# Performance work log

Measured on AMD Instinct MI355X. Metric: run time of the kernel, lower is better.

The kernel has to match this reference:

```python
import jax, jax.numpy as jnp
import numpy as np

POS_THR = 0.5
NEG_THR = 0.4
BBOX_STD = np.array([0.1, 0.1, 0.2, 0.2], dtype=np.float32)


def _make_boxes(key, shape, min_sz, max_sz):
    k1, k2, k3, k4 = jax.random.split(key, 4)
    cy = jax.random.uniform(k1, shape, minval=0.2, maxval=0.8)
    cx = jax.random.uniform(k2, shape, minval=0.2, maxval=0.8)
    h = jax.random.uniform(k3, shape, minval=min_sz, maxval=max_sz)
    w = jax.random.uniform(k4, shape, minval=min_sz, maxval=max_sz)
    return jnp.stack([cy - h * 0.5, cx - w * 0.5, cy + h * 0.5, cx + w * 0.5], axis=-1)


def setup_inputs() -> dict:
    key = jax.random.key(0)
    B, G, A = 16, 64, 65536
    kg, ka, kc = jax.random.split(key, 3)
    gt4 = _make_boxes(kg, (B, G), 0.05, 0.4)            # [B,G,4]
    n_valid = 20                                         # first n_valid gts valid, rest pad
    tag = (jnp.arange(G) < n_valid).astype(jnp.float32)
    tag = jnp.broadcast_to(tag, (B, G))
    gt_boxes = jnp.concatenate([gt4, tag[..., None]], axis=-1)          # [B,G,5]
    cls = jax.random.randint(kc, (B, G), 1, 81).astype(jnp.int32)
    gt_class_ids = jnp.stack([cls, tag.astype(jnp.int32)], axis=-1)     # [B,G,2]
    anchors = _make_boxes(ka, (A,), 0.02, 0.5)                          # [A,4]
    return {"gt_boxes": gt_boxes, "gt_class_ids": gt_class_ids, "anchors": anchors}


def _ssd_target(gt_boxes, gt_class_ids, anchors):
    gt = gt_boxes[..., :4]                       # [B,G,4]
    valid = gt_boxes[..., 4] != 0                # [B,G] pad mask (remove_pad equivalent)
    gy1, gx1, gy2, gx2 = (gt[..., i][:, :, None] for i in range(4))  # [B,G,1]
    ay1, ax1, ay2, ax2 = (anchors[:, i][None, None, :] for i in range(4))  # [1,1,A]
    iw = jnp.maximum(0.0, jnp.minimum(gx2, ax2) - jnp.maximum(gx1, ax1))
    ih = jnp.maximum(0.0, jnp.minimum(gy2, ay2) - jnp.maximum(gy1, ay1))
    inter = iw * ih                              # [B,G,A]
    area_gt = (gx2 - gx1) * (gy2 - gy1)
    area_an = (ax2 - ax1) * (ay2 - ay1)
    iou = inter / (area_gt + area_an - inter)    # [B,G,A]
    iou = jnp.where(valid[:, :, None], iou, -1.0)

    iou_max = jnp.max(iou, axis=1)               # [B,A]
    match_idx = jnp.argmax(iou, axis=1)          # [B,A]
    match_gt = jnp.take_along_axis(gt, match_idx[:, :, None], axis=1)   # [B,A,4]
    class_ids = jnp.take_along_axis(gt_class_ids[..., 0], match_idx, axis=1)  # [B,A]

    anchors_tag = jnp.where(iou_max >= POS_THR, 1.0,
                            jnp.where(iou_max < NEG_THR, -1.0, 0.0))    # [B,A]

    h = anchors[:, 2] - anchors[:, 0]            # [A]
    w = anchors[:, 3] - anchors[:, 1]
    cy = (anchors[:, 2] + anchors[:, 0]) * 0.5
    cx = (anchors[:, 3] + anchors[:, 1]) * 0.5
    gh = match_gt[..., 2] - match_gt[..., 0]     # [B,A]
    gw = match_gt[..., 3] - match_gt[..., 1]
    gcy = (match_gt[..., 2] + match_gt[..., 0]) * 0.5
    gcx = (match_gt[..., 3] + match_gt[..., 1]) * 0.5
    dy = (gcy - cy) / h
    dx = (gcx - cx) / w
    dh = jnp.log(gh / h)
    dw = jnp.log(gw / w)
    deltas = jnp.stack([dy, dx, dh, dw], axis=-1) / jnp.asarray(BBOX_STD)  # [B,A,4]
    return deltas, class_ids, anchors_tag


def reference(gt_boxes, gt_class_ids, anchors):
    return _ssd_target(gt_boxes, gt_class_ids, anchors)
```

## Files before the change

### kernel.cpp

```cpp
#include <hip/hip_runtime.h>

#define G 64
#define POS_THR 0.5f
#define NEG_THR 0.4f

__global__ __launch_bounds__(256) void ssd_target_kernel(
    const float* __restrict__ gt_boxes,
    const int*   __restrict__ gt_class,
    const float* __restrict__ anchors,
    float* __restrict__ out,
    int A, int B)
{
    __shared__ float4 s_box[G];
    __shared__ float  s_area[G], s_cls[G];
    __shared__ int    s_nv;

    const int b = blockIdx.y;
    const int a = blockIdx.x * blockDim.x + threadIdx.x;

    if (threadIdx.x < G) {
        const int g = threadIdx.x;
        const float* p = gt_boxes + ((size_t)b * G + g) * 5;
        const float y1 = p[0], x1 = p[1], y2 = p[2], x2 = p[3], tag = p[4];
        const bool valid = (tag != 0.0f);
        const unsigned long long m = __ballot(valid);
        const int pos = __popcll(m & ((1ull << g) - 1ull));
        const float cls = (float)gt_class[((size_t)b * G + g) * 2 + 0];
        if (valid) {
            s_box[pos] = make_float4(y1, x1, y2, x2);
            s_area[pos] = (x2 - x1) * (y2 - y1);
            s_cls[pos]  = cls;
        }
        if (g == 0) {
            s_nv = __popcll(m);
            if (m == 0ull) {
                s_box[0] = make_float4(y1, x1, y2, x2);
                s_cls[0] = cls;
            }
        }
    }
    __syncthreads();

    if (a >= A) return;

    const float4 an = reinterpret_cast<const float4*>(anchors)[a];
    const float ay1 = an.x, ax1 = an.y, ay2 = an.z, ax2 = an.w;
    const float area_an = (ax2 - ax1) * (ay2 - ay1);
    const int nv = s_nv;

    float best_a = -1.0f, second_a = -1.0f;
    int bestg = 0;
    #pragma unroll 4
    for (int i = 0; i < nv; ++i) {
        const float4 gb = s_box[i];
        float iw = fmaxf(0.0f, fminf(gb.w, ax2) - fmaxf(gb.y, ax1));
        float ih = fmaxf(0.0f, fminf(gb.z, ay2) - fmaxf(gb.x, ay1));
        float inter = iw * ih;
        float denom = s_area[i] + area_an - inter;
        float apx = inter * __builtin_amdgcn_rcpf(denom);
        bestg = (apx > best_a) ? i : bestg;
        second_a = fmaxf(second_a, fminf(apx, best_a));
        best_a = fmaxf(best_a, apx);
    }

    const bool need_exact = (best_a > 0.0f) && (second_a >= best_a * (1.0f - 1e-5f));

    float q;
    int win = bestg;
    if (nv == 0) {
        q = -1.0f;
        win = 0;
    } else if (need_exact) {
        float be = -1.0f; int bi = 0;
        for (int i = 0; i < nv; ++i) {
            const float4 gb = s_box[i];
            float iw = fmaxf(0.0f, fminf(gb.w, ax2) - fmaxf(gb.y, ax1));
            float ih = fmaxf(0.0f, fminf(gb.z, ay2) - fmaxf(gb.x, ay1));
            float inter = iw * ih;
            float denom = s_area[i] + area_an - inter;
            float iou = inter / denom;
            if (iou > be) { be = iou; bi = i; }
        }
        q = be; win = bi;
    } else {
        const float4 gb = s_box[win];
        float iw = fmaxf(0.0f, fminf(gb.w, ax2) - fmaxf(gb.y, ax1));
        float ih = fmaxf(0.0f, fminf(gb.z, ay2) - fmaxf(gb.x, ay1));
        float inter = iw * ih;
        float denom = s_area[win] + area_an - inter;
        q = inter / denom;
    }

    const float4 gw_box = s_box[win];
    const float gy1 = gw_box.x, gx1 = gw_box.y, gy2 = gw_box.z, gx2 = gw_box.w;

    const float h  = ay2 - ay1;
    const float w  = ax2 - ax1;
    const float cy = (ay2 + ay1) * 0.5f;
    const float cx = (ax2 + ax1) * 0.5f;
    const float gh  = gy2 - gy1;
    const float gw  = gx2 - gx1;
    const float gcy = (gy2 + gy1) * 0.5f;
    const float gcx = (gx2 + gx1) * 0.5f;

    const float dy = ((gcy - cy) / h) / 0.1f;
    const float dx = ((gcx - cx) / w) / 0.1f;
    const float dh = logf(gh / h) / 0.2f;
    const float dw = logf(gw / w) / 0.2f;

    const float tag = (q >= POS_THR) ? 1.0f : ((q < NEG_THR) ? -1.0f : 0.0f);

    const size_t idx = (size_t)b * A + a;
    float4 d; d.x = dy; d.y = dx; d.z = dh; d.w = dw;
    reinterpret_cast<float4*>(out)[idx] = d;
    out[(size_t)B * A * 4 + idx] = s_cls[win];
    out[(size_t)B * A * 5 + idx] = tag;
}

extern "C" void kernel_launch(void* const* d_in, const int* in_sizes, int n_in,
                              void* d_out, int out_size, void* d_ws, size_t ws_size,
                              hipStream_t stream) {
    const float* gt_boxes = (const float*)d_in[0];
    const int*   gt_class = (const int*)d_in[1];
    const float* anchors  = (const float*)d_in[2];
    float* out = (float*)d_out;

    const int B = in_sizes[0] / (G * 5);
    const int A = in_sizes[2] / 4;

    dim3 grid(A / 256, B);
    dim3 block(256);
    ssd_target_kernel<<<grid, block, 0, stream>>>(gt_boxes, gt_class, anchors, out, A, B);
}
```

Measured before the change: 79.45 us.

## Process four anchors per thread to reuse shared-memory GT loads

Each thread now handles four anchors, so every GT box read from shared memory is reused across four IoU computations. The grid shrinks by four to match, which also amortizes the per-block GT staging. The epilogue swaps the divisions and logf for hardware reciprocal and fast log2 scaled by constants, which may change rounding slightly in the deltas. The bounds check on a is removed, so the kernel assumes A is divisible by 1024.

```diff
diff --git a/kernel.cpp b/kernel.cpp
--- a/kernel.cpp
+++ b/kernel.cpp
@@ -1,6 +1,7 @@
 #include <hip/hip_runtime.h>
 
 #define G 64
+#define K 4
 #define POS_THR 0.5f
 #define NEG_THR 0.4f
 
@@ -16,13 +17,12 @@
     __shared__ int    s_nv;
 
     const int b = blockIdx.y;
-    const int a = blockIdx.x * blockDim.x + threadIdx.x;
 
     if (threadIdx.x < G) {
         const int g = threadIdx.x;
         const float* p = gt_boxes + ((size_t)b * G + g) * 5;
-        const float y1 = p[0], x1 = p[1], y2 = p[2], x2 = p[3], tag = p[4];
-        const bool valid = (tag != 0.0f);
+        const float y1 = p[0], x1 = p[1], y2 = p[2], x2 = p[3], tagv = p[4];
+        const bool valid = (tagv != 0.0f);
         const unsigned long long m = __ballot(valid);
         const int pos = __popcll(m & ((1ull << g) - 1ull));
         const float cls = (float)gt_class[((size_t)b * G + g) * 2 + 0];
@@ -41,80 +41,97 @@
     }
     __syncthreads();
 
-    if (a >= A) return;
+    const int t  = threadIdx.x;
+    const int a0 = blockIdx.x * (256 * K) + t;
 
-    const float4 an = reinterpret_cast<const float4*>(anchors)[a];
-    const float ay1 = an.x, ax1 = an.y, ay2 = an.z, ax2 = an.w;
-    const float area_an = (ax2 - ax1) * (ay2 - ay1);
+    float4 an[K];
+    float  area_an[K];
+    #pragma unroll
+    for (int k = 0; k < K; ++k) {
+        an[k] = reinterpret_cast<const float4*>(anchors)[a0 + k * 256];
+        area_an[k] = (an[k].w - an[k].y) * (an[k].z - an[k].x);
+    }
+
     const int nv = s_nv;
+    float best[K], second[K];
+    int   bg[K];
+    #pragma unroll
+    for (int k = 0; k < K; ++k) { best[k] = -1.0f; second[k] = -1.0f; bg[k] = 0; }
 
-    float best_a = -1.0f, second_a = -1.0f;
-    int bestg = 0;
-    #pragma unroll 4
+    #pragma unroll 2
     for (int i = 0; i < nv; ++i) {
         const float4 gb = s_box[i];
-        float iw = fmaxf(0.0f, fminf(gb.w, ax2) - fmaxf(gb.y, ax1));
-        float ih = fmaxf(0.0f, fminf(gb.z, ay2) - fmaxf(gb.x, ay1));
-        float inter = iw * ih;
-        float denom = s_area[i] + area_an - inter;
-        float apx = inter * __builtin_amdgcn_rcpf(denom);
-        bestg = (apx > best_a) ? i : bestg;
-        second_a = fmaxf(second_a, fminf(apx, best_a));
-        best_a = fmaxf(best_a, apx);
+        const float  ga = s_area[i];
+        #pragma unroll
+        for (int k = 0; k < K; ++k) {
+            float iw = fmaxf(0.0f, fminf(gb.w, an[k].w) - fmaxf(gb.y, an[k].y));
+            float ih = fmaxf(0.0f, fminf(gb.z, an[k].z) - fmaxf(gb.x, an[k].x));
+            float inter = iw * ih;
+            float denom = ga + area_an[k] - inter;
+            float apx = inter * __builtin_amdgcn_rcpf(denom);
+            bg[k]     = (apx > best[k]) ? i : bg[k];
+            second[k] = fmaxf(second[k], fminf(apx, best[k]));
+            best[k]   = fmaxf(best[k], apx);
+        }
     }
 
-    const bool need_exact = (best_a > 0.0f) && (second_a >= best_a * (1.0f - 1e-5f));
+    #pragma unroll
+    for (int k = 0; k < K; ++k) {
+        const float ay1 = an[k].x, ax1 = an[k].y, ay2 = an[k].z, ax2 = an[k].w;
+        int   win = bg[k];
+        float q;
+        if (nv == 0) {
+            q = -1.0f; win = 0;
+        } else {
+            const bool need_exact =
+                (best[k] > 0.0f) && (second[k] >= best[k] * (1.0f - 1e-5f));
+            if (need_exact) {
+                float be = -1.0f; int bi = 0;
+                for (int i = 0; i < nv; ++i) {
+                    const float4 gb = s_box[i];
+                    float iw = fmaxf(0.0f, fminf(gb.w, ax2) - fmaxf(gb.y, ax1));
+                    float ih = fmaxf(0.0f, fminf(gb.z, ay2) - fmaxf(gb.x, ay1));
+                    float inter = iw * ih;
+                    float denom = s_area[i] + area_an[k] - inter;
+                    float iou = inter / denom;
+                    if (iou > be) { be = iou; bi = i; }
+                }
+                q = be; win = bi;
+            } else {
+                const float4 gb = s_box[win];
+                float iw = fmaxf(0.0f, fminf(gb.w, ax2) - fmaxf(gb.y, ax1));
+                float ih = fmaxf(0.0f, fminf(gb.z, ay2) - fmaxf(gb.x, ay1));
+                float inter = iw * ih;
+                float denom = s_area[win] + area_an[k] - inter;
+                q = inter / denom;
+            }
+        }
 
-    float q;
-    int win = bestg;
-    if (nv == 0) {
-        q = -1.0f;
-        win = 0;
-    } else if (need_exact) {
-        float be = -1.0f; int bi = 0;
-        for (int i = 0; i < nv; ++i) {
-            const float4 gb = s_box[i];
-            float iw = fmaxf(0.0f, fminf(gb.w, ax2) - fmaxf(gb.y, ax1));
-            float ih = fmaxf(0.0f, fminf(gb.z, ay2) - fmaxf(gb.x, ay1));
-            float inter = iw * ih;
-            float denom = s_area[i] + area_an - inter;
-            float iou = inter / denom;
-            if (iou > be) { be = iou; bi = i; }
-        }
-        q = be; win = bi;
-    } else {
         const float4 gb = s_box[win];
-        float iw = fmaxf(0.0f, fminf(gb.w, ax2) - fmaxf(gb.y, ax1));
-        float ih = fmaxf(0.0f, fminf(gb.z, ay2) - fmaxf(gb.x, ay1));
-        float inter = iw * ih;
-        float denom = s_area[win] + area_an - inter;
-        q = inter / denom;
+        const float h  = ay2 - ay1;
+        const float w  = ax2 - ax1;
+        const float rh = __builtin_amdgcn_rcpf(h);
+        const float rw = __builtin_amdgcn_rcpf(w);
+        const float cy = (ay2 + ay1) * 0.5f;
+        const float cx = (ax2 + ax1) * 0.5f;
+        const float gh  = gb.z - gb.x;
+        const float gw  = gb.w - gb.y;
+        const float gcy = (gb.z + gb.x) * 0.5f;
+        const float gcx = (gb.w + gb.y) * 0.5f;
+
+        const float dy = (gcy - cy) * rh * 10.0f;
+        const float dx = (gcx - cx) * rw * 10.0f;
+        const float dh = __log2f(gh * rh) * 3.4657359028f;
+        const float dw = __log2f(gw * rw) * 3.4657359028f;
+
+        const float tag = (q >= POS_THR) ? 1.0f : ((q < NEG_THR) ? -1.0f : 0.0f);
+
+        const size_t idx = (size_t)b * A + (size_t)(a0 + k * 256);
+        float4 d; d.x = dy; d.y = dx; d.z = dh; d.w = dw;
+        reinterpret_cast<float4*>(out)[idx] = d;
+        out[(size_t)B * A * 4 + idx] = s_cls[win];
+        out[(size_t)B * A * 5 + idx] = tag;
     }
-
-    const float4 gw_box = s_box[win];
-    const float gy1 = gw_box.x, gx1 = gw_box.y, gy2 = gw_box.z, gx2 = gw_box.w;
-
-    const float h  = ay2 - ay1;
-    const float w  = ax2 - ax1;
-    const float cy = (ay2 + ay1) * 0.5f;
-    const float cx = (ax2 + ax1) * 0.5f;
-    const float gh  = gy2 - gy1;
-    const float gw  = gx2 - gx1;
-    const float gcy = (gy2 + gy1) * 0.5f;
-    const float gcx = (gx2 + gx1) * 0.5f;
-
-    const float dy = ((gcy - cy) / h) / 0.1f;
-    const float dx = ((gcx - cx) / w) / 0.1f;
-    const float dh = logf(gh / h) / 0.2f;
-    const float dw = logf(gw / w) / 0.2f;
-
-    const float tag = (q >= POS_THR) ? 1.0f : ((q < NEG_THR) ? -1.0f : 0.0f);
-
-    const size_t idx = (size_t)b * A + a;
-    float4 d; d.x = dy; d.y = dx; d.z = dh; d.w = dw;
-    reinterpret_cast<float4*>(out)[idx] = d;
-    out[(size_t)B * A * 4 + idx] = s_cls[win];
-    out[(size_t)B * A * 5 + idx] = tag;
 }
 
 extern "C" void kernel_launch(void* const* d_in, const int* in_sizes, int n_in,
@@ -128,7 +145,7 @@
     const int B = in_sizes[0] / (G * 5);
     const int A = in_sizes[2] / 4;
 
-    dim3 grid(A / 256, B);
+    dim3 grid(A / (256 * K), B);
     dim3 block(256);
     ssd_target_kernel<<<grid, block, 0, stream>>>(gt_boxes, gt_class, anchors, out, A, B);
 }
```

New measurement: 78.68 us. No clear change (-1.0%).
